# Optimization experiments

Hardware: AMD Instinct MI355X
Metric: run time of the kernel (lower is better)

## Reference

```python
import jax, jax.numpy as jnp
import numpy as np

N_NODES = 100_000
N_EDGES = 1_600_000
D_IN = 128
D_HID = 128
LN_EPS = 1e-5


def setup_inputs() -> dict:
    key = jax.random.key(0)
    k1, k2, k3 = jax.random.split(key, 3)
    x = jax.random.normal(k1, (N_NODES, D_IN), dtype=jnp.float32)
    edge_index = jax.random.randint(k2, (2, N_EDGES), 0, N_NODES, dtype=jnp.int32)
    # GCNConv linear weight (glorot-ish) and bias
    W = jax.random.normal(k3, (D_IN, D_HID), dtype=jnp.float32) * (1.0 / np.sqrt(D_IN))
    b = jnp.zeros((D_HID,), dtype=jnp.float32)
    # LayerNorm params
    gamma = jnp.ones((D_HID,), dtype=jnp.float32)
    beta = jnp.zeros((D_HID,), dtype=jnp.float32)
    return {"x": x, "edge_index": edge_index, "W": W, "b": b, "gamma": gamma, "beta": beta}


def reference(x, edge_index, W, b, gamma, beta):
    n = x.shape[0]
    # --- GCNConv: add self-loops, symmetric normalization ---
    loop = jnp.arange(n, dtype=edge_index.dtype)
    row = jnp.concatenate([edge_index[0], loop])  # source j
    col = jnp.concatenate([edge_index[1], loop])  # target i
    deg = jax.ops.segment_sum(jnp.ones(row.shape, x.dtype), col, num_segments=n)
    dinv = jnp.where(deg > 0, jax.lax.rsqrt(deg), jnp.zeros_like(deg))
    norm = dinv[row] * dinv[col]  # [E+N]
    # transform first (input->hidden), then gather-scale-scatter
    h = x @ W  # [N, D_HID]
    msg = h[row] * norm[:, None]  # gather + per-edge scale
    out = jax.ops.segment_sum(msg, col, num_segments=n) + b  # scatter-add
    # --- LayerNorm ---
    mu = jnp.mean(out, axis=-1, keepdims=True)
    var = jnp.mean(jnp.square(out - mu), axis=-1, keepdims=True)
    ln = (out - mu) * jax.lax.rsqrt(var + LN_EPS) * gamma + beta
    # Dropout is identity at inference; ReLU
    return jax.nn.relu(ln)
```

## Files before the change

kernel.cpp:

```cpp
#include <hip/hip_runtime.h>
#include <hip/hip_bf16.h>
#include <math.h>

#define LN_EPS 1e-5f
#define CAP 2048
#define CAPSH 11
#define SIDXSZ (CAP + 448)
#define NPBLK 128
#define MAXBUCK 1600

typedef __attribute__((ext_vector_type(8))) short short8;
typedef __attribute__((ext_vector_type(4))) float floatx4;

__global__ __launch_bounds__(256) void k_init(const float* __restrict__ W, __hip_bfloat16* __restrict__ Wt,
                                              int* __restrict__ bucketCnt, unsigned* __restrict__ gdummy,
                                              float* __restrict__ dinv, int N) {
    int t = threadIdx.x;
    int i = blockIdx.x * 256 + t;
    int n = i >> 7, k = i & 127;
    Wt[i] = __float2bfloat16(W[k * 128 + n]);
    if (blockIdx.x == 0) {
        for (int j = t; j < MAXBUCK; j += 256) bucketCnt[j] = 0;
        if (t < 64) gdummy[t] = 0;
        if (t == 0) dinv[N] = 0.f;
    }
}

__global__ __launch_bounds__(256) void k_part_gemm(const int* __restrict__ ei, int* __restrict__ bucketCnt,
                                                   unsigned* __restrict__ pk, int E, int chunk,
                                                   const float* __restrict__ x, const __hip_bfloat16* __restrict__ Wt,
                                                   __hip_bfloat16* __restrict__ g, int N) {
    __shared__ union {
        struct { int h[MAXBUCK]; int base[MAXBUCK]; } part;
        unsigned short sB[128 * 128];
    } u;
    if ((int)blockIdx.x < NPBLK) {
        int t = threadIdx.x;
        for (int i = t; i < MAXBUCK; i += 256) u.part.h[i] = 0;
        int e0 = blockIdx.x * chunk;
        int e1 = min(e0 + chunk, E);
        __syncthreads();
        for (int i = e0 + t; i < e1; i += 256)
            atomicAdd(&u.part.h[ei[E + i] >> 6], 1);
        __syncthreads();
        for (int i = t; i < MAXBUCK; i += 256) {
            if (u.part.h[i] > 0) {
                u.part.base[i] = atomicAdd(&bucketCnt[i], u.part.h[i]);
                u.part.h[i] = 0;
            }
        }
        __syncthreads();
        for (int i = e0 + t; i < e1; i += 256) {
            int col = ei[E + i];
            int src = ei[i];
            int b = col >> 6;
            int r = u.part.base[b] + atomicAdd(&u.part.h[b], 1);
            if (r < CAP)
                pk[((unsigned)b << CAPSH) + r] = ((unsigned)(col & 63) << 20) | (unsigned)src;
        }
    } else {
        int tid = threadIdx.x;
        int row0 = ((int)blockIdx.x - NPBLK) * 128;
#pragma unroll
        for (int i = 0; i < 8; ++i) {
            int idx = tid + i * 256;
            int row = idx >> 4;
            int gr = idx & 15;
            int grs = gr ^ (row & 15);
            *(short8*)(&u.sB[row * 128 + grs * 8]) = *(const short8*)(Wt + (size_t)row * 128 + gr * 8);
        }
        __syncthreads();
        int lane = tid & 63;
        int wv = tid >> 6;
        int m = lane & 15;
        int q = lane >> 4;
        floatx4 acc[2][8];
#pragma unroll
        for (int mt = 0; mt < 2; ++mt)
#pragma unroll
            for (int nt = 0; nt < 8; ++nt) acc[mt][nt] = (floatx4){0.f, 0.f, 0.f, 0.f};
#pragma unroll
        for (int kc = 0; kc < 4; ++kc) {
            int gg = kc * 4 + q;
            short8 afrag[2], bfrag[8];
#pragma unroll
            for (int mt = 0; mt < 2; ++mt) {
                int arow = min(row0 + wv * 32 + mt * 16 + m, N - 1);
                const float* xp = x + (size_t)arow * 128 + gg * 8;
                float4 xa = *(const float4*)xp;
                float4 xb = *(const float4*)(xp + 4);
                union { short8 s; __hip_bfloat16 h[8]; } a;
                a.h[0] = __float2bfloat16(xa.x); a.h[1] = __float2bfloat16(xa.y);
                a.h[2] = __float2bfloat16(xa.z); a.h[3] = __float2bfloat16(xa.w);
                a.h[4] = __float2bfloat16(xb.x); a.h[5] = __float2bfloat16(xb.y);
                a.h[6] = __float2bfloat16(xb.z); a.h[7] = __float2bfloat16(xb.w);
                afrag[mt] = a.s;
            }
#pragma unroll
            for (int nt = 0; nt < 8; ++nt) {
                int n = nt * 16 + m;
                bfrag[nt] = *(const short8*)(&u.sB[n * 128 + (gg ^ (n & 15)) * 8]);
            }
#pragma unroll
            for (int mt = 0; mt < 2; ++mt)
#pragma unroll
                for (int nt = 0; nt < 8; ++nt)
                    acc[mt][nt] = __builtin_amdgcn_mfma_f32_16x16x32_bf16(afrag[mt], bfrag[nt], acc[mt][nt], 0, 0, 0);
        }
#pragma unroll
        for (int mt = 0; mt < 2; ++mt) {
#pragma unroll
            for (int i = 0; i < 4; ++i) {
                int row = row0 + wv * 32 + mt * 16 + q * 4 + i;
                if (row < N) {
                    __hip_bfloat16* gp = g + (size_t)row * 128;
#pragma unroll
                    for (int nt = 0; nt < 8; ++nt)
                        gp[nt * 16 + m] = __float2bfloat16(acc[mt][nt][i]);
                }
            }
        }
    }
}

__global__ __launch_bounds__(256) void k_deg(const unsigned* __restrict__ pk, const int* __restrict__ bucketCnt,
                                             int* __restrict__ cnt, float* __restrict__ dinv, int N) {
    __shared__ int lc[64];
    int b = blockIdx.x;
    int t = threadIdx.x;
    if (t < 64) lc[t] = 0;
    __syncthreads();
    int ofs = b << CAPSH;
    int cntb = min(bucketCnt[b], CAP);
    for (int e = t; e < cntb; e += 256)
        atomicAdd(&lc[pk[ofs + e] >> 20], 1);
    __syncthreads();
    int node = (b << 6) + t;
    if (t < 64 && node < N) {
        cnt[node] = lc[t];
        dinv[node] = rsqrtf((float)(lc[t] + 1));
    }
}

#define RLF(V, I) __int_as_float(__builtin_amdgcn_readlane(__float_as_int(V), (I)))

#define LOAD8(P, B) \
    unsigned P##0 = g1[((size_t)(unsigned)__builtin_amdgcn_readlane(myidx, (B) + 0)) * 64u + lane]; \
    unsigned P##1 = g1[((size_t)(unsigned)__builtin_amdgcn_readlane(myidx, (B) + 1)) * 64u + lane]; \
    unsigned P##2 = g1[((size_t)(unsigned)__builtin_amdgcn_readlane(myidx, (B) + 2)) * 64u + lane]; \
    unsigned P##3 = g1[((size_t)(unsigned)__builtin_amdgcn_readlane(myidx, (B) + 3)) * 64u + lane]; \
    unsigned P##4 = g1[((size_t)(unsigned)__builtin_amdgcn_readlane(myidx, (B) + 4)) * 64u + lane]; \
    unsigned P##5 = g1[((size_t)(unsigned)__builtin_amdgcn_readlane(myidx, (B) + 5)) * 64u + lane]; \
    unsigned P##6 = g1[((size_t)(unsigned)__builtin_amdgcn_readlane(myidx, (B) + 6)) * 64u + lane]; \
    unsigned P##7 = g1[((size_t)(unsigned)__builtin_amdgcn_readlane(myidx, (B) + 7)) * 64u + lane];

#define WACC8(P, B) { \
    float w0 = RLF(dlv, (B) + 0), w1 = RLF(dlv, (B) + 1), w2 = RLF(dlv, (B) + 2), w3 = RLF(dlv, (B) + 3); \
    float w4 = RLF(dlv, (B) + 4), w5 = RLF(dlv, (B) + 5), w6 = RLF(dlv, (B) + 6), w7 = RLF(dlv, (B) + 7); \
    ax += ((__uint_as_float(P##0 << 16) * w0 + __uint_as_float(P##1 << 16) * w1) + \
           (__uint_as_float(P##2 << 16) * w2 + __uint_as_float(P##3 << 16) * w3)) + \
          ((__uint_as_float(P##4 << 16) * w4 + __uint_as_float(P##5 << 16) * w5) + \
           (__uint_as_float(P##6 << 16) * w6 + __uint_as_float(P##7 << 16) * w7)); \
    ay += ((__uint_as_float(P##0 & 0xFFFF0000u) * w0 + __uint_as_float(P##1 & 0xFFFF0000u) * w1) + \
           (__uint_as_float(P##2 & 0xFFFF0000u) * w2 + __uint_as_float(P##3 & 0xFFFF0000u) * w3)) + \
          ((__uint_as_float(P##4 & 0xFFFF0000u) * w4 + __uint_as_float(P##5 & 0xFFFF0000u) * w5) + \
           (__uint_as_float(P##6 & 0xFFFF0000u) * w6 + __uint_as_float(P##7 & 0xFFFF0000u) * w7)); }

__global__ __launch_bounds__(256) void k_agg_ln(const __hip_bfloat16* __restrict__ g, const unsigned* __restrict__ pk,
                                                const int* __restrict__ bucketCnt, const int* __restrict__ cnt,
                                                const float* __restrict__ dinv, const float* __restrict__ bias,
                                                const float* __restrict__ gamma, const float* __restrict__ beta,
                                                float* __restrict__ out, int N) {
    __shared__ int sidx[SIDXSZ];
    __shared__ int sscan[256];
    __shared__ int lofs[64];
    __shared__ int pvs[64];
    __shared__ int lcnt[64];
    int b = blockIdx.x;
    int t = threadIdx.x;
    int ofs = b << CAPSH;
    int cntb = min(bucketCnt[b], CAP);
    int nd = (b << 6) + t;
    int v = (t < 64 && nd < N) ? cnt[nd] : 0;
    int pv = (v + 7) & ~7;
    sscan[t] = pv;
    __syncthreads();
    int val = pv;
    for (int off = 1; off < 256; off <<= 1) {
        int add = (t >= off) ? sscan[t - off] : 0;
        __syncthreads();
        val += add;
        sscan[t] = val;
        __syncthreads();
    }
    if (t < 64) {
        int base = val - pv;
        lofs[t] = base;
        pvs[t] = pv;
        lcnt[t] = 0;
        for (int i = v; i < pv; ++i) {
            int sl = base + i;
            if (sl < SIDXSZ) sidx[sl] = N;
        }
    }
    __syncthreads();
    for (int e = t; e < cntb; e += 256) {
        unsigned u = pk[ofs + e];
        int d = u >> 20;
        int r = atomicAdd(&lcnt[d], 1);
        int sl = lofs[d] + r;
        if (sl < SIDXSZ) sidx[sl] = (int)(u & 0xFFFFFu);
    }
    __syncthreads();
    int lane = t & 63;
    int wv = t >> 6;
    const unsigned* g1 = (const unsigned*)g;
    float2 bi = ((const float2*)bias)[lane];
    float2 ga = ((const float2*)gamma)[lane];
    float2 be = ((const float2*)beta)[lane];
    for (int ii = 0; ii < 16; ++ii) {
        int nl = wv * 16 + ii;
        int node = (b << 6) + nl;
        if (node >= N) break;
        int startL = lofs[nl];
        int endL = startL + pvs[nl];
        float di = dinv[node];
        unsigned sv = g1[(size_t)node * 64 + lane];
        float ax = __uint_as_float(sv << 16) * di;
        float ay = __uint_as_float(sv & 0xFFFF0000u) * di;
        for (int eb = startL; eb < endL; eb += 64) {
            int myidx = (eb + lane < endL) ? sidx[eb + lane] : N;
            float dlv = dinv[myidx];
            int nb = min(64, endL - eb);
            if (nb >= 24) {
                LOAD8(pa, 0)
                LOAD8(pb, 8)
                LOAD8(pc, 16)
                WACC8(pa, 0)
                WACC8(pb, 8)
                WACC8(pc, 16)
                for (int j = 24; j + 8 <= nb; j += 8) {
                    LOAD8(pd, j)
                    WACC8(pd, j)
                }
            } else if (nb == 16) {
                LOAD8(pe, 0)
                LOAD8(pf, 8)
                WACC8(pe, 0)
                WACC8(pf, 8)
            } else {
                LOAD8(pg, 0)
                WACC8(pg, 0)
            }
        }
        float vx = ax * di + bi.x;
        float vy = ay * di + bi.y;
        float sum = vx + vy, sq = vx * vx + vy * vy;
#pragma unroll
        for (int off = 32; off > 0; off >>= 1) {
            sum += __shfl_xor(sum, off, 64);
            sq += __shfl_xor(sq, off, 64);
        }
        float mu = sum * (1.0f / 128.0f);
        float var = sq * (1.0f / 128.0f) - mu * mu;
        float rstd = rsqrtf(var + LN_EPS);
        float o0 = fmaxf((vx - mu) * rstd * ga.x + be.x, 0.f);
        float o1 = fmaxf((vy - mu) * rstd * ga.y + be.y, 0.f);
        ((float2*)out)[(size_t)node * 64 + lane] = make_float2(o0, o1);
    }
}

extern "C" void kernel_launch(void* const* d_in, const int* in_sizes, int n_in,
                              void* d_out, int out_size, void* d_ws, size_t ws_size,
                              hipStream_t stream) {
    const float* x = (const float*)d_in[0];
    const int* ei = (const int*)d_in[1];
    const float* W = (const float*)d_in[2];
    const float* bias = (const float*)d_in[3];
    const float* gamma = (const float*)d_in[4];
    const float* beta = (const float*)d_in[5];
    float* out = (float*)d_out;

    int N = in_sizes[0] / 128;
    int E = in_sizes[1] / 2;
    int NBUCK = (N + 63) / 64;

    char* p = (char*)d_ws;
    auto alloc = [&](size_t bytes) {
        char* r = p;
        p += (bytes + 255) & ~(size_t)255;
        return r;
    };
    int* bucketCnt = (int*)alloc(MAXBUCK * 4);
    int* cnt = (int*)alloc((size_t)N * 4);
    float* dinv = (float*)alloc((size_t)(N + 1) * 4);
    __hip_bfloat16* Wt = (__hip_bfloat16*)alloc(128 * 128 * 2);
    unsigned* pk = (unsigned*)alloc((size_t)NBUCK * CAP * 4);
    __hip_bfloat16* gbuf = (__hip_bfloat16*)alloc((size_t)(N + 1) * 128 * 2);

    int chunk = (E + NPBLK - 1) / NPBLK;
    int GB = (N + 127) / 128;

    k_init<<<64, 256, 0, stream>>>(W, Wt, bucketCnt, (unsigned*)(gbuf + (size_t)N * 128), dinv, N);
    k_part_gemm<<<NPBLK + GB, 256, 0, stream>>>(ei, bucketCnt, pk, E, chunk, x, Wt, gbuf, N);
    k_deg<<<NBUCK, 256, 0, stream>>>(pk, bucketCnt, cnt, dinv, N);
    k_agg_ln<<<NBUCK, 256, 0, stream>>>(gbuf, pk, bucketCnt, cnt, dinv, bias, gamma, beta, out, N);
}
```

Measured before the change: 249.0 us.

## Drop init kernel, stage edges in LDS, widen partitioning grid, use wave-shuffle scan

Removes the k_init kernel: W is transposed and converted to bf16 directly into shared memory inside the GEMM blocks, bucket counters are cleared with a memset, and the dummy row and dinv sentinel are zeroed in k_deg. The partition phase now runs on many more blocks with small chunks and caches each chunk's edge columns and sources in LDS, so edge_index is read from global memory once instead of twice. The aggregation kernel replaces its 256-wide block scan, with its many barriers, by a single-wave shuffle scan. In exchange, every GEMM block re-reads and converts the fp32 W with scattered 2-byte LDS writes, and the larger partition grid issues more global atomics on the bucket counters.

New measurement: 223.7 us. 1.11x faster.

```diff
diff --git a/kernel.cpp b/kernel.cpp
--- a/kernel.cpp
+++ b/kernel.cpp
@@ -6,32 +6,19 @@
 #define CAP 2048
 #define CAPSH 11
 #define SIDXSZ (CAP + 448)
-#define NPBLK 128
+#define NPBLK 667
+#define ECHUNK 2400
 #define MAXBUCK 1600
 
 typedef __attribute__((ext_vector_type(8))) short short8;
 typedef __attribute__((ext_vector_type(4))) float floatx4;
 
-__global__ __launch_bounds__(256) void k_init(const float* __restrict__ W, __hip_bfloat16* __restrict__ Wt,
-                                              int* __restrict__ bucketCnt, unsigned* __restrict__ gdummy,
-                                              float* __restrict__ dinv, int N) {
-    int t = threadIdx.x;
-    int i = blockIdx.x * 256 + t;
-    int n = i >> 7, k = i & 127;
-    Wt[i] = __float2bfloat16(W[k * 128 + n]);
-    if (blockIdx.x == 0) {
-        for (int j = t; j < MAXBUCK; j += 256) bucketCnt[j] = 0;
-        if (t < 64) gdummy[t] = 0;
-        if (t == 0) dinv[N] = 0.f;
-    }
-}
-
 __global__ __launch_bounds__(256) void k_part_gemm(const int* __restrict__ ei, int* __restrict__ bucketCnt,
                                                    unsigned* __restrict__ pk, int E, int chunk,
-                                                   const float* __restrict__ x, const __hip_bfloat16* __restrict__ Wt,
+                                                   const float* __restrict__ x, const float* __restrict__ W,
                                                    __hip_bfloat16* __restrict__ g, int N) {
     __shared__ union {
-        struct { int h[MAXBUCK]; int base[MAXBUCK]; } part;
+        struct { int ecol[ECHUNK]; int esrc[ECHUNK]; int h[MAXBUCK]; int base[MAXBUCK]; } part;
         unsigned short sB[128 * 128];
     } u;
     if ((int)blockIdx.x < NPBLK) {
@@ -39,9 +26,14 @@
         for (int i = t; i < MAXBUCK; i += 256) u.part.h[i] = 0;
         int e0 = blockIdx.x * chunk;
         int e1 = min(e0 + chunk, E);
+        int n = e1 - e0;
         __syncthreads();
-        for (int i = e0 + t; i < e1; i += 256)
-            atomicAdd(&u.part.h[ei[E + i] >> 6], 1);
+        for (int i = t; i < n; i += 256) {
+            int col = ei[E + e0 + i];
+            u.part.ecol[i] = col;
+            u.part.esrc[i] = ei[e0 + i];
+            atomicAdd(&u.part.h[col >> 6], 1);
+        }
         __syncthreads();
         for (int i = t; i < MAXBUCK; i += 256) {
             if (u.part.h[i] > 0) {
@@ -50,24 +42,27 @@
             }
         }
         __syncthreads();
-        for (int i = e0 + t; i < e1; i += 256) {
-            int col = ei[E + i];
-            int src = ei[i];
+        for (int i = t; i < n; i += 256) {
+            int col = u.part.ecol[i];
             int b = col >> 6;
             int r = u.part.base[b] + atomicAdd(&u.part.h[b], 1);
             if (r < CAP)
-                pk[((unsigned)b << CAPSH) + r] = ((unsigned)(col & 63) << 20) | (unsigned)src;
+                pk[((unsigned)b << CAPSH) + r] = ((unsigned)(col & 63) << 20) | (unsigned)u.part.esrc[i];
         }
     } else {
         int tid = threadIdx.x;
         int row0 = ((int)blockIdx.x - NPBLK) * 128;
 #pragma unroll
-        for (int i = 0; i < 8; ++i) {
-            int idx = tid + i * 256;
-            int row = idx >> 4;
-            int gr = idx & 15;
-            int grs = gr ^ (row & 15);
-            *(short8*)(&u.sB[row * 128 + grs * 8]) = *(const short8*)(Wt + (size_t)row * 128 + gr * 8);
+        for (int i = 0; i < 16; ++i) {
+            int qd = tid + i * 256;
+            int k = qd >> 5;
+            int n0 = (qd & 31) * 4;
+            float4 w = *(const float4*)(W + (size_t)k * 128 + n0);
+            int gq = k >> 3, kj = k & 7;
+            u.sB[(n0 + 0) * 128 + ((gq ^ ((n0 + 0) & 15)) << 3) + kj] = (unsigned short)(__bfloat16_as_ushort(__float2bfloat16(w.x)));
+            u.sB[(n0 + 1) * 128 + ((gq ^ ((n0 + 1) & 15)) << 3) + kj] = (unsigned short)(__bfloat16_as_ushort(__float2bfloat16(w.y)));
+            u.sB[(n0 + 2) * 128 + ((gq ^ ((n0 + 2) & 15)) << 3) + kj] = (unsigned short)(__bfloat16_as_ushort(__float2bfloat16(w.z)));
+            u.sB[(n0 + 3) * 128 + ((gq ^ ((n0 + 3) & 15)) << 3) + kj] = (unsigned short)(__bfloat16_as_ushort(__float2bfloat16(w.w)));
         }
         __syncthreads();
         int lane = tid & 63;
@@ -99,7 +94,7 @@
 #pragma unroll
             for (int nt = 0; nt < 8; ++nt) {
                 int n = nt * 16 + m;
-                bfrag[nt] = *(const short8*)(&u.sB[n * 128 + (gg ^ (n & 15)) * 8]);
+                bfrag[nt] = *(const short8*)(&u.sB[n * 128 + ((gg ^ (n & 15)) << 3)]);
             }
 #pragma unroll
             for (int mt = 0; mt < 2; ++mt)
@@ -124,11 +119,16 @@
 }
 
 __global__ __launch_bounds__(256) void k_deg(const unsigned* __restrict__ pk, const int* __restrict__ bucketCnt,
-                                             int* __restrict__ cnt, float* __restrict__ dinv, int N) {
+                                             int* __restrict__ cnt, float* __restrict__ dinv,
+                                             unsigned* __restrict__ gdummy, int N) {
     __shared__ int lc[64];
     int b = blockIdx.x;
     int t = threadIdx.x;
     if (t < 64) lc[t] = 0;
+    if (b == 0) {
+        if (t >= 128 && t < 192) gdummy[t - 128] = 0;
+        if (t == 192) dinv[N] = 0.f;
+    }
     __syncthreads();
     int ofs = b << CAPSH;
     int cntb = min(bucketCnt[b], CAP);
@@ -172,32 +172,29 @@
                                                 const float* __restrict__ gamma, const float* __restrict__ beta,
                                                 float* __restrict__ out, int N) {
     __shared__ int sidx[SIDXSZ];
-    __shared__ int sscan[256];
     __shared__ int lofs[64];
     __shared__ int pvs[64];
     __shared__ int lcnt[64];
     int b = blockIdx.x;
     int t = threadIdx.x;
+    int lane = t & 63;
+    int wv = t >> 6;
     int ofs = b << CAPSH;
     int cntb = min(bucketCnt[b], CAP);
-    int nd = (b << 6) + t;
-    int v = (t < 64 && nd < N) ? cnt[nd] : 0;
-    int pv = (v + 7) & ~7;
-    sscan[t] = pv;
-    __syncthreads();
-    int val = pv;
-    for (int off = 1; off < 256; off <<= 1) {
-        int add = (t >= off) ? sscan[t - off] : 0;
-        __syncthreads();
-        val += add;
-        sscan[t] = val;
-        __syncthreads();
-    }
     if (t < 64) {
+        int nd = (b << 6) + lane;
+        int v = (nd < N) ? cnt[nd] : 0;
+        int pv = (v + 7) & ~7;
+        int val = pv;
+#pragma unroll
+        for (int off = 1; off < 64; off <<= 1) {
+            int o = __shfl_up(val, off, 64);
+            if (lane >= off) val += o;
+        }
         int base = val - pv;
-        lofs[t] = base;
-        pvs[t] = pv;
-        lcnt[t] = 0;
+        lofs[lane] = base;
+        pvs[lane] = pv;
+        lcnt[lane] = 0;
         for (int i = v; i < pv; ++i) {
             int sl = base + i;
             if (sl < SIDXSZ) sidx[sl] = N;
@@ -212,8 +209,6 @@
         if (sl < SIDXSZ) sidx[sl] = (int)(u & 0xFFFFFu);
     }
     __syncthreads();
-    int lane = t & 63;
-    int wv = t >> 6;
     const unsigned* g1 = (const unsigned*)g;
     float2 bi = ((const float2*)bias)[lane];
     float2 ga = ((const float2*)gamma)[lane];
@@ -294,15 +289,14 @@
     int* bucketCnt = (int*)alloc(MAXBUCK * 4);
     int* cnt = (int*)alloc((size_t)N * 4);
     float* dinv = (float*)alloc((size_t)(N + 1) * 4);
-    __hip_bfloat16* Wt = (__hip_bfloat16*)alloc(128 * 128 * 2);
     unsigned* pk = (unsigned*)alloc((size_t)NBUCK * CAP * 4);
     __hip_bfloat16* gbuf = (__hip_bfloat16*)alloc((size_t)(N + 1) * 128 * 2);
 
     int chunk = (E + NPBLK - 1) / NPBLK;
     int GB = (N + 127) / 128;
 
-    k_init<<<64, 256, 0, stream>>>(W, Wt, bucketCnt, (unsigned*)(gbuf + (size_t)N * 128), dinv, N);
-    k_part_gemm<<<NPBLK + GB, 256, 0, stream>>>(ei, bucketCnt, pk, E, chunk, x, Wt, gbuf, N);
-    k_deg<<<NBUCK, 256, 0, stream>>>(pk, bucketCnt, cnt, dinv, N);
+    hipMemsetAsync(bucketCnt, 0, MAXBUCK * 4, stream);
+    k_part_gemm<<<NPBLK + GB, 256, 0, stream>>>(ei, bucketCnt, pk, E, chunk, x, W, gbuf, N);
+    k_deg<<<NBUCK, 256, 0, stream>>>(pk, bucketCnt, cnt, dinv, (unsigned*)(gbuf + (size_t)N * 128), N);
     k_agg_ln<<<NBUCK, 256, 0, stream>>>(gbuf, pk, bucketCnt, cnt, dinv, bias, gamma, beta, out, N);
 }
```
